# Performance work log

Hardware: AMD Instinct MI355X
Metric: run time of the kernel (lower is better)

Reference implementation:

```python
import jax, jax.numpy as jnp
import numpy as np

D_MODEL = 1024
N_HEADS = 16
HEAD_DIM = D_MODEL // N_HEADS


def setup_inputs() -> dict:
    key = jax.random.key(0)
    kx, kq, kk, kv, ko = jax.random.split(key, 5)
    B, T = 2, 2048
    # nn.Linear(d_model, d_model, bias=False) weights, stored as [out, in] like torch
    s = 1.0 / np.sqrt(D_MODEL)
    x = jax.random.normal(kx, (B, T, D_MODEL), dtype=jnp.float32)
    Wq = jax.random.uniform(kq, (D_MODEL, D_MODEL), minval=-s, maxval=s, dtype=jnp.float32)
    Wk = jax.random.uniform(kk, (D_MODEL, D_MODEL), minval=-s, maxval=s, dtype=jnp.float32)
    Wv = jax.random.uniform(kv, (D_MODEL, D_MODEL), minval=-s, maxval=s, dtype=jnp.float32)
    Wo = jax.random.uniform(ko, (D_MODEL, D_MODEL), minval=-s, maxval=s, dtype=jnp.float32)
    return {"x": x, "Wq": Wq, "Wk": Wk, "Wv": Wv, "Wo": Wo}


def reference(x, Wq, Wk, Wv, Wo):
    B, T, C = x.shape
    H, Dh = N_HEADS, HEAD_DIM
    # projections (torch Linear: x @ W.T)
    q = (x @ Wq.T).reshape(B, T, H, Dh).transpose(0, 2, 1, 3)  # [B,H,T,Dh]
    k = (x @ Wk.T).reshape(B, T, H, Dh).transpose(0, 2, 1, 3)
    v = (x @ Wv.T).reshape(B, T, H, Dh).transpose(0, 2, 1, 3)
    scores = jnp.einsum('bhqd,bhkd->bhqk', q, k) / jnp.sqrt(jnp.float32(Dh))
    causal = jnp.tril(jnp.ones((T, T), dtype=bool))  # [T,T]
    scores = jnp.where(causal[None, None], scores, -jnp.inf)
    attn = jax.nn.softmax(scores, axis=-1)
    out = jnp.einsum('bhqk,bhkd->bhqd', attn, v)  # [B,H,T,Dh]
    out = out.transpose(0, 2, 1, 3).reshape(B, T, C)
    return out @ Wo.T
```

## Files before the change

kernel.cpp:

```cpp
#include <hip/hip_runtime.h>
#include <hip/hip_bf16.h>

#define BB 2
#define TT 2048
#define CC 1024
#define HH 16
#define DH 64

typedef __attribute__((ext_vector_type(8))) short bf16x8;
typedef __attribute__((ext_vector_type(4))) float f32x4;
using bf16 = __hip_bfloat16;

union cvt8u { bf16x8 v; bf16 b[8]; };

__device__ __forceinline__ bf16x8 load8(const bf16* p) {
    return *reinterpret_cast<const bf16x8*>(p);
}

__device__ __forceinline__ bf16x8 cvt8f(const float* p) {
    const float4 a = *reinterpret_cast<const float4*>(p);
    const float4 c = *reinterpret_cast<const float4*>(p + 4);
    cvt8u u;
    u.b[0] = __float2bfloat16(a.x); u.b[1] = __float2bfloat16(a.y);
    u.b[2] = __float2bfloat16(a.z); u.b[3] = __float2bfloat16(a.w);
    u.b[4] = __float2bfloat16(c.x); u.b[5] = __float2bfloat16(c.y);
    u.b[6] = __float2bfloat16(c.z); u.b[7] = __float2bfloat16(c.w);
    return u.v;
}

__device__ __forceinline__ f32x4 mfma16(bf16x8 a, bf16x8 b, f32x4 c) {
    return __builtin_amdgcn_mfma_f32_16x16x32_bf16(a, b, c, 0, 0, 0);
}

__device__ __forceinline__ void gload_lds16(const bf16* g, bf16* l) {
    __builtin_amdgcn_global_load_lds(
        (const __attribute__((address_space(1))) void*)g,
        (__attribute__((address_space(3))) void*)l, 16, 0, 0);
}

#define QSCALE (0.125f * 1.44269504088896f)


__global__ __launch_bounds__(256) void cvt_x(const float* __restrict__ in,
                                             bf16* __restrict__ out) {
    const int i = blockIdx.x * 256 + threadIdx.x;
    *(reinterpret_cast<bf16x8*>(out) + i) = cvt8f(in + (size_t)i * 8);
}

__global__ __launch_bounds__(256) void cvt4_w(const float* __restrict__ w0,
                                              const float* __restrict__ w1,
                                              const float* __restrict__ w2,
                                              const float* __restrict__ w3,
                                              bf16* __restrict__ out) {
    const float* in = (blockIdx.y == 0) ? w0 : (blockIdx.y == 1) ? w1
                    : (blockIdx.y == 2) ? w2 : w3;
    const int i = blockIdx.x * 256 + threadIdx.x;
    bf16* o = out + (size_t)blockIdx.y * CC * CC;
    *(reinterpret_cast<bf16x8*>(o) + i) = cvt8f(in + (size_t)i * 8);
}

template <int MODE>
__global__ __launch_bounds__(256) void gemm3(const bf16* __restrict__ A,
                                             const bf16* __restrict__ B,
                                             bf16* __restrict__ oq,
                                             bf16* __restrict__ ok,
                                             bf16* __restrict__ ov,
                                             float* __restrict__ outf) {
    __shared__ __align__(16) bf16 As[128 * 32];
    __shared__ __align__(16) bf16 Bs[128 * 32];
    const int lane = threadIdx.x & 63;
    const int wv = threadIdx.x >> 6;
    const int l15 = lane & 15;
    const int g = lane >> 4;
    const int m0 = blockIdx.x * 128;
    const int n0 = blockIdx.y * 128;

    const int srow = wv * 16 + (lane >> 2);
    const int skg = (lane & 3) * 8;
    const bf16* gA0 = A + (size_t)(m0 + srow) * CC + skg;
    const bf16* gA1 = A + (size_t)(m0 + 64 + srow) * CC + skg;
    const bf16* gB0 = B + (size_t)(n0 + srow) * CC + skg;
    const bf16* gB1 = B + (size_t)(n0 + 64 + srow) * CC + skg;
    bf16* lA0 = As + wv * 512;
    bf16* lA1 = As + 2048 + wv * 512;
    bf16* lB0 = Bs + wv * 512;
    bf16* lB1 = Bs + 2048 + wv * 512;

    const int mw = (wv >> 1) * 64;
    const int nw = (wv & 1) * 64;

    f32x4 acc[4][4] = {};

    for (int kk = 0; kk < CC; kk += 32) {
        __syncthreads();
        gload_lds16(gA0 + kk, lA0);
        gload_lds16(gA1 + kk, lA1);
        gload_lds16(gB0 + kk, lB0);
        gload_lds16(gB1 + kk, lB1);
        __syncthreads();

        bf16x8 af[4], wf[4];
#pragma unroll
        for (int mi = 0; mi < 4; mi++)
            af[mi] = load8(As + (mw + mi * 16 + l15) * 32 + g * 8);
#pragma unroll
        for (int ni = 0; ni < 4; ni++)
            wf[ni] = load8(Bs + (nw + ni * 16 + l15) * 32 + g * 8);
#pragma unroll
        for (int mi = 0; mi < 4; mi++)
#pragma unroll
            for (int ni = 0; ni < 4; ni++)
                acc[mi][ni] = mfma16(af[mi], wf[ni], acc[mi][ni]);
    }

#pragma unroll
    for (int mi = 0; mi < 4; mi++) {
#pragma unroll
        for (int ni = 0; ni < 4; ni++) {
            const int n = n0 + nw + ni * 16 + l15;
#pragma unroll
            for (int r = 0; r < 4; r++) {
                const int m = m0 + mw + mi * 16 + g * 4 + r;
                const float v = acc[mi][ni][r];
                if (MODE == 1) {
                    outf[(size_t)m * CC + n] = v;
                } else {
                    const int b = m >> 11, t = m & (TT - 1);
                    const int mat = n >> 10, nn = n & 1023;
                    const int h = nn >> 6, d = nn & 63;
                    if (mat == 0) {
                        oq[((size_t)((b * HH + h) * TT + t) << 6) + d] = __float2bfloat16(v * QSCALE);
                    } else if (mat == 1) {
                        ok[((size_t)((b * HH + h) * TT + t) << 6) + d] = __float2bfloat16(v);
                    } else {
                        ov[(size_t)((b * HH + h) * DH + d) * TT + ((t + (d << 6)) & (TT - 1))] = __float2bfloat16(v);
                    }
                }
            }
        }
    }
}

template <int MODE>
__global__ __launch_bounds__(256) void gemm2(const bf16* __restrict__ A,
                                             const float* __restrict__ W0,
                                             const float* __restrict__ W1,
                                             const float* __restrict__ W2,
                                             bf16* __restrict__ oq,
                                             bf16* __restrict__ ok,
                                             bf16* __restrict__ ov,
                                             float* __restrict__ outf) {
    const int lane = threadIdx.x & 63;
    const int wv = threadIdx.x >> 6;
    const int l15 = lane & 15;
    const int g = lane >> 4;
    const int mw = blockIdx.x * 128 + (wv >> 1) * 64;
    const int nw = blockIdx.y * 128 + (wv & 1) * 64;

    f32x4 acc[4][4] = {};

    const bf16* ap[4];
#pragma unroll
    for (int mi = 0; mi < 4; mi++)
        ap[mi] = A + (size_t)(mw + mi * 16 + l15) * CC + g * 8;

    const float* wfp[4];
#pragma unroll
    for (int ni = 0; ni < 4; ni++) {
        const int nt = nw + ni * 16;
        const float* base = (MODE == 1) ? W0
                          : (nt < 1024) ? W0 : (nt < 2048) ? W1 : W2;
        wfp[ni] = base + (size_t)((nt & 1023) + l15) * CC + g * 8;
    }

#pragma unroll 2
    for (int kk = 0; kk < CC; kk += 32) {
        bf16x8 af[4], wf[4];
#pragma unroll
        for (int mi = 0; mi < 4; mi++) af[mi] = load8(ap[mi] + kk);
#pragma unroll
        for (int ni = 0; ni < 4; ni++) wf[ni] = cvt8f(wfp[ni] + kk);
#pragma unroll
        for (int mi = 0; mi < 4; mi++)
#pragma unroll
            for (int ni = 0; ni < 4; ni++)
                acc[mi][ni] = mfma16(af[mi], wf[ni], acc[mi][ni]);
    }

#pragma unroll
    for (int mi = 0; mi < 4; mi++) {
#pragma unroll
        for (int ni = 0; ni < 4; ni++) {
            const int n = nw + ni * 16 + l15;
#pragma unroll
            for (int r = 0; r < 4; r++) {
                const int m = mw + mi * 16 + g * 4 + r;
                const float v = acc[mi][ni][r];
                if (MODE == 1) {
                    outf[(size_t)m * CC + n] = v;
                } else {
                    const int b = m >> 11, t = m & (TT - 1);
                    const int mat = n >> 10, nn = n & 1023;
                    const int h = nn >> 6, d = nn & 63;
                    if (mat == 0) {
                        oq[((size_t)((b * HH + h) * TT + t) << 6) + d] = __float2bfloat16(v * QSCALE);
                    } else if (mat == 1) {
                        ok[((size_t)((b * HH + h) * TT + t) << 6) + d] = __float2bfloat16(v);
                    } else {
                        ov[(size_t)((b * HH + h) * DH + d) * TT + ((t + (d << 6)) & (TT - 1))] = __float2bfloat16(v);
                    }
                }
            }
        }
    }
}

__global__ __launch_bounds__(128, 2) void attn_v10(const bf16* __restrict__ Q,
                                                   const bf16* __restrict__ K,
                                                   const bf16* __restrict__ Vt,
                                                   bf16* __restrict__ out) {
    __shared__ __align__(16) bf16 p_lds[2][2][16 * 72];
    __shared__ __align__(16) float o_cmb[2][4][64][4];
    __shared__ float l_cmb[2][16];
    const int lane = threadIdx.x & 63;
    const int wv = threadIdx.x >> 6;
    const int l15 = lane & 15;
    const int g = lane >> 4;

    const int bid = blockIdx.x;
    const int xcd = bid & 7;
    const int idx = bid >> 3;
    const int bh = xcd * 4 + (idx >> 6);
    const int c = idx & 63;

    const int qbA = c * 16;
    const int qbB = (127 - c) * 16;
    const int nkbA = (c >> 2) + 1;
    const int nkbB = ((127 - c) >> 2) + 1;

    const bf16* Qh = Q + (size_t)bh * TT * DH;
    const bf16* Kh = K + (size_t)bh * TT * DH;
    const bf16* Vh = Vt + (size_t)bh * DH * TT;

    const bf16x8 qa0 = load8(Qh + (size_t)(qbA + l15) * DH + g * 8);
    const bf16x8 qa1 = load8(Qh + (size_t)(qbA + l15) * DH + 32 + g * 8);
    const bf16x8 qb0 = load8(Qh + (size_t)(qbB + l15) * DH + g * 8);
    const bf16x8 qb1 = load8(Qh + (size_t)(qbB + l15) * DH + 32 + g * 8);

    f32x4 oA[4] = {}, oB[4] = {};
    float lA[4] = {0.0f, 0.0f, 0.0f, 0.0f};
    float lB[4] = {0.0f, 0.0f, 0.0f, 0.0f};

    bf16* plA = p_lds[wv][0];
    bf16* plB = p_lds[wv][1];

    bf16x8 kf0[4], kf1[4];
#pragma unroll
    for (int j = 0; j < 4; j++) {
        kf0[j] = load8(Kh + (size_t)(wv * 64 + j * 16 + l15) * DH + g * 8);
        kf1[j] = load8(Kh + (size_t)(wv * 64 + j * 16 + l15) * DH + 32 + g * 8);
    }

    for (int kb = wv; kb < nkbB; kb += 2) {
        const int k0 = kb * 64;
        const bool actA = (kb < nkbA);

        f32x4 SA[4] = {}, SB[4] = {};
        if (actA) {
#pragma unroll
            for (int j = 0; j < 4; j++) {
                SA[j] = mfma16(qa0, kf0[j], SA[j]);
                SA[j] = mfma16(qa1, kf1[j], SA[j]);
            }
        }
#pragma unroll
        for (int j = 0; j < 4; j++) {
            SB[j] = mfma16(qb0, kf0[j], SB[j]);
            SB[j] = mfma16(qb1, kf1[j], SB[j]);
        }

        bf16x8 vf0[4], vf1[4];
#pragma unroll
        for (int dt = 0; dt < 4; dt++) {
            const int d0 = dt * 16 + l15;
            const int sk = (d0 << 6);
            vf0[dt] = load8(Vh + (size_t)d0 * TT + ((k0 + g * 8 + sk) & (TT - 1)));
            vf1[dt] = load8(Vh + (size_t)d0 * TT + ((k0 + 32 + g * 8 + sk) & (TT - 1)));
        }

        if (kb + 2 < nkbB) {
            const int kn = k0 + 128;
#pragma unroll
            for (int j = 0; j < 4; j++) {
                kf0[j] = load8(Kh + (size_t)(kn + j * 16 + l15) * DH + g * 8);
                kf1[j] = load8(Kh + (size_t)(kn + j * 16 + l15) * DH + 32 + g * 8);
            }
        }

        if (actA && kb == nkbA - 1) {
#pragma unroll
            for (int j = 0; j < 4; j++)
#pragma unroll
                for (int r = 0; r < 4; r++)
                    if (k0 + j * 16 + l15 > qbA + g * 4 + r) SA[j][r] = -1e30f;
        }
        if (kb == nkbB - 1) {
#pragma unroll
            for (int j = 0; j < 4; j++)
#pragma unroll
                for (int r = 0; r < 4; r++)
                    if (k0 + j * 16 + l15 > qbB + g * 4 + r) SB[j][r] = -1e30f;
        }

        float PA[4][4], PB[4][4];
        if (actA) {
#pragma unroll
            for (int r = 0; r < 4; r++)
#pragma unroll
                for (int j = 0; j < 4; j++) {
                    PA[j][r] = exp2f(SA[j][r]);
                    lA[r] += PA[j][r];
                }
        }
#pragma unroll
        for (int r = 0; r < 4; r++)
#pragma unroll
            for (int j = 0; j < 4; j++) {
                PB[j][r] = exp2f(SB[j][r]);
                lB[r] += PB[j][r];
            }

        if (actA) {
#pragma unroll
            for (int j = 0; j < 4; j++)
#pragma unroll
                for (int r = 0; r < 4; r++)
                    plA[(g * 4 + r) * 72 + j * 16 + l15] = __float2bfloat16(PA[j][r]);
        }
#pragma unroll
        for (int j = 0; j < 4; j++)
#pragma unroll
            for (int r = 0; r < 4; r++)
                plB[(g * 4 + r) * 72 + j * 16 + l15] = __float2bfloat16(PB[j][r]);
        asm volatile("s_waitcnt lgkmcnt(0)" ::: "memory");

        const bf16x8 pb0 = load8(plB + l15 * 72 + g * 8);
        const bf16x8 pb1 = load8(plB + l15 * 72 + 32 + g * 8);
#pragma unroll
        for (int dt = 0; dt < 4; dt++) {
            oB[dt] = mfma16(pb0, vf0[dt], oB[dt]);
            oB[dt] = mfma16(pb1, vf1[dt], oB[dt]);
        }
        if (actA) {
            const bf16x8 pa0 = load8(plA + l15 * 72 + g * 8);
            const bf16x8 pa1 = load8(plA + l15 * 72 + 32 + g * 8);
#pragma unroll
            for (int dt = 0; dt < 4; dt++) {
                oA[dt] = mfma16(pa0, vf0[dt], oA[dt]);
                oA[dt] = mfma16(pa1, vf1[dt], oA[dt]);
            }
        }
    }

#pragma unroll
    for (int xm = 1; xm < 16; xm <<= 1) {
#pragma unroll
        for (int r = 0; r < 4; r++) {
            lA[r] += __shfl_xor(lA[r], xm);
            lB[r] += __shfl_xor(lB[r], xm);
        }
    }

    if (wv == 1) {
#pragma unroll
        for (int dt = 0; dt < 4; dt++) {
            *reinterpret_cast<f32x4*>(&o_cmb[0][dt][lane][0]) = oA[dt];
            *reinterpret_cast<f32x4*>(&o_cmb[1][dt][lane][0]) = oB[dt];
        }
        if (l15 == 0) {
#pragma unroll
            for (int r = 0; r < 4; r++) {
                l_cmb[0][g * 4 + r] = lA[r];
                l_cmb[1][g * 4 + r] = lB[r];
            }
        }
    }
    __syncthreads();
    if (wv == 1) return;

#pragma unroll
    for (int dt = 0; dt < 4; dt++) {
        oA[dt] += *reinterpret_cast<const f32x4*>(&o_cmb[0][dt][lane][0]);
        oB[dt] += *reinterpret_cast<const f32x4*>(&o_cmb[1][dt][lane][0]);
    }
#pragma unroll
    for (int r = 0; r < 4; r++) {
        lA[r] += l_cmb[0][g * 4 + r];
        lB[r] += l_cmb[1][g * 4 + r];
    }

    const int b = bh >> 4, h = bh & 15;
#pragma unroll
    for (int r = 0; r < 4; r++) {
        const float invA = 1.0f / lA[r];
        const float invB = 1.0f / lB[r];
        const int tA = qbA + g * 4 + r;
        const int tB = qbB + g * 4 + r;
        bf16* opA = out + (size_t)(b * TT + tA) * CC + h * DH;
        bf16* opB = out + (size_t)(b * TT + tB) * CC + h * DH;
#pragma unroll
        for (int dt = 0; dt < 4; dt++) {
            opA[dt * 16 + l15] = __float2bfloat16(oA[dt][r] * invA);
            opB[dt * 16 + l15] = __float2bfloat16(oB[dt][r] * invB);
        }
    }
}

extern "C" void kernel_launch(void* const* d_in, const int* in_sizes, int n_in,
                              void* d_out, int out_size, void* d_ws, size_t ws_size,
                              hipStream_t stream) {
    const float* x  = (const float*)d_in[0];
    const float* Wq = (const float*)d_in[1];
    const float* Wk = (const float*)d_in[2];
    const float* Wv = (const float*)d_in[3];
    const float* Wo = (const float*)d_in[4];
    float* out = (float*)d_out;

    const size_t per = (size_t)BB * HH * TT * DH;
    bf16* Qws  = (bf16*)d_ws;
    bf16* Kws  = Qws + per;
    bf16* Vtws = Kws + per;
    bf16* xbf  = Vtws + per;
    bf16* attn = xbf;
    bf16* Wball = attn + per;
    const bool full = ws_size >= 5 * per * sizeof(bf16);

    const dim3 blk(256);
    cvt_x<<<dim3(2048), blk, 0, stream>>>(x, xbf);

    if (full) {
        cvt4_w<<<dim3(512, 4), blk, 0, stream>>>(Wq, Wk, Wv, Wo, Wball);
        gemm3<0><<<dim3(32, 24), blk, 0, stream>>>(
            xbf, Wball, Qws, Kws, Vtws, nullptr);
    } else {
        gemm2<0><<<dim3(32, 24), blk, 0, stream>>>(
            xbf, Wq, Wk, Wv, Qws, Kws, Vtws, nullptr);
    }

    attn_v10<<<dim3(2048), dim3(128), 0, stream>>>(Qws, Kws, Vtws, attn);

    if (full) {
        gemm3<1><<<dim3(32, 8), blk, 0, stream>>>(
            attn, Wball + (size_t)3 * CC * CC, nullptr, nullptr, nullptr, out);
    } else {
        gemm2<1><<<dim3(32, 8), blk, 0, stream>>>(
            attn, Wo, nullptr, nullptr, nullptr, nullptr, nullptr, out);
    }
}
```

Baseline: 242.0 us.

## Split paired query tiles into one tile per block, doubling grid

The attention kernel used to pair a short causal query tile with its mirrored long tile in one block, sharing K/V fragment loads between them. It now gives each block a single 16-row query tile and launches twice as many blocks, lowering per-block register and LDS use. This can raise occupancy and simplify control flow. In exchange, K/V loads are no longer shared between two tiles and per-block work becomes uneven across the causal triangle, so load balance depends on the hardware scheduler.

```diff
diff --git a/kernel.cpp b/kernel.cpp
--- a/kernel.cpp
+++ b/kernel.cpp
@@ -215,13 +215,13 @@
     }
 }
 
-__global__ __launch_bounds__(128, 2) void attn_v10(const bf16* __restrict__ Q,
+__global__ __launch_bounds__(128, 2) void attn_v11(const bf16* __restrict__ Q,
                                                    const bf16* __restrict__ K,
                                                    const bf16* __restrict__ Vt,
                                                    bf16* __restrict__ out) {
-    __shared__ __align__(16) bf16 p_lds[2][2][16 * 72];
-    __shared__ __align__(16) float o_cmb[2][4][64][4];
-    __shared__ float l_cmb[2][16];
+    __shared__ __align__(16) bf16 p_lds[2][16 * 72];
+    __shared__ __align__(16) float o_cmb[4][64][4];
+    __shared__ float l_cmb[16];
     const int lane = threadIdx.x & 63;
     const int wv = threadIdx.x >> 6;
     const int l15 = lane & 15;
@@ -230,29 +230,23 @@
     const int bid = blockIdx.x;
     const int xcd = bid & 7;
     const int idx = bid >> 3;
-    const int bh = xcd * 4 + (idx >> 6);
-    const int c = idx & 63;
-
-    const int qbA = c * 16;
-    const int qbB = (127 - c) * 16;
-    const int nkbA = (c >> 2) + 1;
-    const int nkbB = ((127 - c) >> 2) + 1;
+    const int bh = xcd * 4 + (idx >> 7);
+    const int c = idx & 127;
+
+    const int qb = c * 16;
+    const int nkb = (c >> 2) + 1;
 
     const bf16* Qh = Q + (size_t)bh * TT * DH;
     const bf16* Kh = K + (size_t)bh * TT * DH;
     const bf16* Vh = Vt + (size_t)bh * DH * TT;
 
-    const bf16x8 qa0 = load8(Qh + (size_t)(qbA + l15) * DH + g * 8);
-    const bf16x8 qa1 = load8(Qh + (size_t)(qbA + l15) * DH + 32 + g * 8);
-    const bf16x8 qb0 = load8(Qh + (size_t)(qbB + l15) * DH + g * 8);
-    const bf16x8 qb1 = load8(Qh + (size_t)(qbB + l15) * DH + 32 + g * 8);
-
-    f32x4 oA[4] = {}, oB[4] = {};
-    float lA[4] = {0.0f, 0.0f, 0.0f, 0.0f};
-    float lB[4] = {0.0f, 0.0f, 0.0f, 0.0f};
-
-    bf16* plA = p_lds[wv][0];
-    bf16* plB = p_lds[wv][1];
+    const bf16x8 q0 = load8(Qh + (size_t)(qb + l15) * DH + g * 8);
+    const bf16x8 q1 = load8(Qh + (size_t)(qb + l15) * DH + 32 + g * 8);
+
+    f32x4 o[4] = {};
+    float l[4] = {0.0f, 0.0f, 0.0f, 0.0f};
+
+    bf16* const pl = p_lds[wv];
 
     bf16x8 kf0[4], kf1[4];
 #pragma unroll
@@ -261,22 +255,14 @@
         kf1[j] = load8(Kh + (size_t)(wv * 64 + j * 16 + l15) * DH + 32 + g * 8);
     }
 
-    for (int kb = wv; kb < nkbB; kb += 2) {
+    for (int kb = wv; kb < nkb; kb += 2) {
         const int k0 = kb * 64;
-        const bool actA = (kb < nkbA);
-
-        f32x4 SA[4] = {}, SB[4] = {};
-        if (actA) {
-#pragma unroll
-            for (int j = 0; j < 4; j++) {
-                SA[j] = mfma16(qa0, kf0[j], SA[j]);
-                SA[j] = mfma16(qa1, kf1[j], SA[j]);
-            }
-        }
+
+        f32x4 S[4] = {};
 #pragma unroll
         for (int j = 0; j < 4; j++) {
-            SB[j] = mfma16(qb0, kf0[j], SB[j]);
-            SB[j] = mfma16(qb1, kf1[j], SB[j]);
+            S[j] = mfma16(q0, kf0[j], S[j]);
+            S[j] = mfma16(q1, kf1[j], S[j]);
         }
 
         bf16x8 vf0[4], vf1[4];
@@ -288,7 +274,7 @@
             vf1[dt] = load8(Vh + (size_t)d0 * TT + ((k0 + 32 + g * 8 + sk) & (TT - 1)));
         }
 
-        if (kb + 2 < nkbB) {
+        if (kb + 2 < nkb) {
             const int kn = k0 + 128;
 #pragma unroll
             for (int j = 0; j < 4; j++) {
@@ -297,122 +283,71 @@
             }
         }
 
-        if (actA && kb == nkbA - 1) {
+        if (kb == nkb - 1) {
 #pragma unroll
             for (int j = 0; j < 4; j++)
 #pragma unroll
                 for (int r = 0; r < 4; r++)
-                    if (k0 + j * 16 + l15 > qbA + g * 4 + r) SA[j][r] = -1e30f;
-        }
-        if (kb == nkbB - 1) {
-#pragma unroll
-            for (int j = 0; j < 4; j++)
-#pragma unroll
-                for (int r = 0; r < 4; r++)
-                    if (k0 + j * 16 + l15 > qbB + g * 4 + r) SB[j][r] = -1e30f;
-        }
-
-        float PA[4][4], PB[4][4];
-        if (actA) {
+                    if (k0 + j * 16 + l15 > qb + g * 4 + r) S[j][r] = -1e30f;
+        }
+
+#pragma unroll
+        for (int r = 0; r < 4; r++)
+#pragma unroll
+            for (int j = 0; j < 4; j++) {
+                S[j][r] = exp2f(S[j][r]);
+                l[r] += S[j][r];
+            }
+
+#pragma unroll
+        for (int j = 0; j < 4; j++)
 #pragma unroll
             for (int r = 0; r < 4; r++)
-#pragma unroll
-                for (int j = 0; j < 4; j++) {
-                    PA[j][r] = exp2f(SA[j][r]);
-                    lA[r] += PA[j][r];
-                }
-        }
-#pragma unroll
-        for (int r = 0; r < 4; r++)
-#pragma unroll
-            for (int j = 0; j < 4; j++) {
-                PB[j][r] = exp2f(SB[j][r]);
-                lB[r] += PB[j][r];
-            }
-
-        if (actA) {
-#pragma unroll
-            for (int j = 0; j < 4; j++)
-#pragma unroll
-                for (int r = 0; r < 4; r++)
-                    plA[(g * 4 + r) * 72 + j * 16 + l15] = __float2bfloat16(PA[j][r]);
-        }
-#pragma unroll
-        for (int j = 0; j < 4; j++)
-#pragma unroll
-            for (int r = 0; r < 4; r++)
-                plB[(g * 4 + r) * 72 + j * 16 + l15] = __float2bfloat16(PB[j][r]);
+                pl[(g * 4 + r) * 72 + j * 16 + l15] = __float2bfloat16(S[j][r]);
         asm volatile("s_waitcnt lgkmcnt(0)" ::: "memory");
 
-        const bf16x8 pb0 = load8(plB + l15 * 72 + g * 8);
-        const bf16x8 pb1 = load8(plB + l15 * 72 + 32 + g * 8);
+        const bf16x8 pf0 = load8(pl + l15 * 72 + g * 8);
+        const bf16x8 pf1 = load8(pl + l15 * 72 + 32 + g * 8);
 #pragma unroll
         for (int dt = 0; dt < 4; dt++) {
-            oB[dt] = mfma16(pb0, vf0[dt], oB[dt]);
-            oB[dt] = mfma16(pb1, vf1[dt], oB[dt]);
-        }
-        if (actA) {
-            const bf16x8 pa0 = load8(plA + l15 * 72 + g * 8);
-            const bf16x8 pa1 = load8(plA + l15 * 72 + 32 + g * 8);
-#pragma unroll
-            for (int dt = 0; dt < 4; dt++) {
-                oA[dt] = mfma16(pa0, vf0[dt], oA[dt]);
-                oA[dt] = mfma16(pa1, vf1[dt], oA[dt]);
-            }
+            o[dt] = mfma16(pf0, vf0[dt], o[dt]);
+            o[dt] = mfma16(pf1, vf1[dt], o[dt]);
         }
     }
 
 #pragma unroll
     for (int xm = 1; xm < 16; xm <<= 1) {
 #pragma unroll
-        for (int r = 0; r < 4; r++) {
-            lA[r] += __shfl_xor(lA[r], xm);
-            lB[r] += __shfl_xor(lB[r], xm);
-        }
+        for (int r = 0; r < 4; r++) l[r] += __shfl_xor(l[r], xm);
     }
 
     if (wv == 1) {
 #pragma unroll
-        for (int dt = 0; dt < 4; dt++) {
-            *reinterpret_cast<f32x4*>(&o_cmb[0][dt][lane][0]) = oA[dt];
-            *reinterpret_cast<f32x4*>(&o_cmb[1][dt][lane][0]) = oB[dt];
-        }
+        for (int dt = 0; dt < 4; dt++)
+            *reinterpret_cast<f32x4*>(&o_cmb[dt][lane][0]) = o[dt];
         if (l15 == 0) {
 #pragma unroll
-            for (int r = 0; r < 4; r++) {
-                l_cmb[0][g * 4 + r] = lA[r];
-                l_cmb[1][g * 4 + r] = lB[r];
-            }
+            for (int r = 0; r < 4; r++) l_cmb[g * 4 + r] = l[r];
         }
     }
     __syncthreads();
     if (wv == 1) return;
 
 #pragma unroll
-    for (int dt = 0; dt < 4; dt++) {
-        oA[dt] += *reinterpret_cast<const f32x4*>(&o_cmb[0][dt][lane][0]);
-        oB[dt] += *reinterpret_cast<const f32x4*>(&o_cmb[1][dt][lane][0]);
-    }
+    for (int dt = 0; dt < 4; dt++)
+        o[dt] += *reinterpret_cast<const f32x4*>(&o_cmb[dt][lane][0]);
+#pragma unroll
+    for (int r = 0; r < 4; r++) l[r] += l_cmb[g * 4 + r];
+
+    const int b = bh >> 4, h = bh & 15;
 #pragma unroll
     for (int r = 0; r < 4; r++) {
-        lA[r] += l_cmb[0][g * 4 + r];
-        lB[r] += l_cmb[1][g * 4 + r];
-    }
-
-    const int b = bh >> 4, h = bh & 15;
-#pragma unroll
-    for (int r = 0; r < 4; r++) {
-        const float invA = 1.0f / lA[r];
-        const float invB = 1.0f / lB[r];
-        const int tA = qbA + g * 4 + r;
-        const int tB = qbB + g * 4 + r;
-        bf16* opA = out + (size_t)(b * TT + tA) * CC + h * DH;
-        bf16* opB = out + (size_t)(b * TT + tB) * CC + h * DH;
-#pragma unroll
-        for (int dt = 0; dt < 4; dt++) {
-            opA[dt * 16 + l15] = __float2bfloat16(oA[dt][r] * invA);
-            opB[dt * 16 + l15] = __float2bfloat16(oB[dt][r] * invB);
-        }
+        const float inv = 1.0f / l[r];
+        const int t = qb + g * 4 + r;
+        bf16* op = out + (size_t)(b * TT + t) * CC + h * DH;
+#pragma unroll
+        for (int dt = 0; dt < 4; dt++)
+            op[dt * 16 + l15] = __float2bfloat16(o[dt][r] * inv);
     }
 }
 
@@ -447,7 +382,7 @@
             xbf, Wq, Wk, Wv, Qws, Kws, Vtws, nullptr);
     }
 
-    attn_v10<<<dim3(2048), dim3(128), 0, stream>>>(Qws, Kws, Vtws, attn);
+    attn_v11<<<dim3(4096), dim3(128), 0, stream>>>(Qws, Kws, Vtws, attn);
 
     if (full) {
         gemm3<1><<<dim3(32, 8), blk, 0, stream>>>(
```

Result: slower. 283.1 us (+17.0%).
